# Kernel optimization log

Measured on AMD Instinct MI355X. Metric: run time of the kernel, lower is better.

The kernel has to match this reference:

```python
import jax, jax.numpy as jnp
import numpy as np

N_NODES = 100000
F_IN = 512
HIDDEN = 64
N_CLASS = 40
N_EDGES = 3200000


def gcn_conv(x, src, dst, deg_inv_sqrt, W, b, n_nodes):
    # PyG GCNConv: linear transform, then deg^{-1/2} A_hat deg^{-1/2} aggregation, then bias
    h = x @ W  # [N, out]
    norm = deg_inv_sqrt[src] * deg_inv_sqrt[dst]  # [E+N] (includes self-loops)
    msg = h[src] * norm[:, None]  # gather + scale
    out = jax.ops.segment_sum(msg, dst, num_segments=n_nodes)  # scatter-add
    return out + b


def setup_inputs() -> dict:
    key = jax.random.key(0)
    k1, k2, k3, k4, k5 = jax.random.split(key, 5)
    x = jax.random.normal(k1, (N_NODES, F_IN), dtype=jnp.float32)
    edge_index = jax.random.randint(k2, (2, N_EDGES), 0, N_NODES, dtype=jnp.int64)
    # Glorot-style init for GCN weights
    W1 = jax.random.normal(k3, (F_IN, HIDDEN), dtype=jnp.float32) / np.sqrt(F_IN)
    b1 = jnp.zeros((HIDDEN,), dtype=jnp.float32)
    W2 = jax.random.normal(k4, (HIDDEN, N_CLASS), dtype=jnp.float32) / np.sqrt(HIDDEN)
    b2 = jnp.zeros((N_CLASS,), dtype=jnp.float32)
    return {"x": x, "edge_index": edge_index, "W1": W1, "b1": b1, "W2": W2, "b2": b2}


def reference(x, edge_index, W1, b1, W2, b2):
    n = x.shape[0]
    loops = jnp.arange(n, dtype=edge_index.dtype)
    src = jnp.concatenate([edge_index[0], loops])  # add self-loops (GCNConv default)
    dst = jnp.concatenate([edge_index[1], loops])
    deg = jax.ops.segment_sum(jnp.ones_like(dst, dtype=x.dtype), dst, num_segments=n)
    deg_inv_sqrt = jnp.where(deg > 0, jax.lax.rsqrt(deg), 0.0)
    h = gcn_conv(x, src, dst, deg_inv_sqrt, W1, b1, n)
    h = jax.nn.relu(h)  # dropout treated as eval-mode identity
    x_out = gcn_conv(h, src, dst, deg_inv_sqrt, W2, b2, n)
    return jax.nn.log_softmax(x_out, axis=1), x_out
```

## Files before the change

### kernel.cpp

```cpp
#include <hip/hip_runtime.h>
#include <math.h>

#define N_NODES 100000
#define F_IN    512
#define HIDDEN  64
#define N_CLASS 40
#define N_EDGES 3200000
#define NB      782
#define CAP     6144
#define EPB     8192
#define NPB     391

typedef int EIdx;

typedef __attribute__((ext_vector_type(8))) short short8;
typedef __attribute__((ext_vector_type(4))) float f32x4;
typedef __attribute__((ext_vector_type(4))) unsigned uint4v;

__device__ inline short f2bf(float f) {
    unsigned u = __builtin_bit_cast(unsigned, f);
    unsigned r = u + 0x7FFFu + ((u >> 16) & 1u);
    return (short)(r >> 16);
}

__device__ inline unsigned cvtpk(float lo, float hi) {
    unsigned r;
    asm("v_cvt_pk_bf16_f32 %0, %1, %2" : "=v"(r) : "v"(lo), "v"(hi));
    return r;
}

__device__ inline float bflo(unsigned w) { return __builtin_bit_cast(float, w << 16); }
__device__ inline float bfhi(unsigned w) { return __builtin_bit_cast(float, w & 0xFFFF0000u); }

__global__ __launch_bounds__(256) void binit_kernel(int* __restrict__ bcur) {
    int i = blockIdx.x * 256 + threadIdx.x;
    if (i < NB) bcur[i] = i * CAP;
}

__global__ __launch_bounds__(256) void part1_kernel(const EIdx* __restrict__ src,
                                                    const EIdx* __restrict__ dst,
                                                    int* __restrict__ bcur,
                                                    unsigned* __restrict__ bpacked) {
    __shared__ int hist[NB];
    __shared__ int excl[NB];
    __shared__ int cur[NB];
    __shared__ int delta[NB];
    __shared__ int stmp[256];
    __shared__ unsigned spk[EPB];
    __shared__ unsigned short bid[EPB];
    int t = threadIdx.x;
    int e0 = blockIdx.x * EPB;
    int dreg[32];
    for (int j = t; j < NB; j += 256) hist[j] = 0;
    __syncthreads();
#pragma unroll
    for (int k = 0; k < 32; ++k) {
        int e = e0 + k * 256 + t;
        dreg[k] = (e < N_EDGES) ? dst[e] : -1;
        if (dreg[k] >= 0) atomicAdd(&hist[dreg[k] >> 7], 1);
    }
    __syncthreads();
    {
        int i0 = 4 * t;
        int v0 = (i0 < NB) ? hist[i0] : 0;
        int v1 = (i0 + 1 < NB) ? hist[i0 + 1] : 0;
        int v2 = (i0 + 2 < NB) ? hist[i0 + 2] : 0;
        int v3 = (i0 + 3 < NB) ? hist[i0 + 3] : 0;
        int s = v0 + v1 + v2 + v3;
        stmp[t] = s;
        __syncthreads();
        for (int o = 1; o < 256; o <<= 1) {
            int a = (t >= o) ? stmp[t - o] : 0;
            __syncthreads();
            stmp[t] += a;
            __syncthreads();
        }
        int E = stmp[t] - s;
        if (i0 < NB) excl[i0] = E;
        if (i0 + 1 < NB) excl[i0 + 1] = E + v0;
        if (i0 + 2 < NB) excl[i0 + 2] = E + v0 + v1;
        if (i0 + 3 < NB) excl[i0 + 3] = E + v0 + v1 + v2;
    }
    __syncthreads();
    for (int j = t; j < NB; j += 256) {
        int h = hist[j];
        int rsv = h ? atomicAdd(&bcur[j], h) : 0;
        delta[j] = rsv - excl[j];
        cur[j] = excl[j];
    }
    __syncthreads();
#pragma unroll
    for (int k = 0; k < 32; ++k) {
        int d = dreg[k];
        if (d >= 0) {
            int e = e0 + k * 256 + t;
            int s = src[e];
            int b = d >> 7;
            int p = atomicAdd(&cur[b], 1);
            spk[p] = ((unsigned)(d & 127) << 20) | (unsigned)s;
            bid[p] = (unsigned short)b;
        }
    }
    __syncthreads();
    int cnt = N_EDGES - e0;
    if (cnt > EPB) cnt = EPB;
    for (int i = t; i < cnt; i += 256) {
        int bb = bid[i];
        int pos = i + delta[bb];
        if (pos < (bb + 1) * CAP) bpacked[pos] = spk[i];
    }
}

__global__ __launch_bounds__(256) void part2_kernel(const int* __restrict__ bcur,
                                                    const unsigned* __restrict__ bpacked,
                                                    int* __restrict__ csr_src,
                                                    unsigned* __restrict__ rowmeta,
                                                    float* __restrict__ dis) {
    __shared__ unsigned ent[CAP];
    __shared__ int hist[128];
    __shared__ int stmp[128];
    __shared__ int cur[128];
    int t = threadIdx.x;
    int bk = blockIdx.x;
    int base = bk * CAP;
    int cnt = bcur[bk] - base;
    if (cnt > CAP) cnt = CAP;
    if (t < 128) hist[t] = 0;
    __syncthreads();
    for (int i = t; i < cnt; i += 256) {
        unsigned p = bpacked[base + i];
        ent[i] = p;
        atomicAdd(&hist[p >> 20], 1);
    }
    __syncthreads();
    if (t < 128) stmp[t] = hist[t];
    __syncthreads();
    for (int o = 1; o < 128; o <<= 1) {
        int a = (t >= o && t < 128) ? stmp[t - o] : 0;
        __syncthreads();
        if (t < 128) stmp[t] += a;
        __syncthreads();
    }
    if (t < 128) {
        int ex = stmp[t] - hist[t];
        cur[t] = ex;
        int n = (bk << 7) + t;
        if (n < N_NODES) {
            rowmeta[n] = (unsigned)(base + ex) | ((unsigned)hist[t] << 23);
            dis[n] = rsqrtf((float)(hist[t] + 1));
        }
    }
    __syncthreads();
    for (int i = t; i < cnt; i += 256) {
        unsigned p = ent[i];
        int p2 = atomicAdd(&cur[p >> 20], 1);
        csr_src[base + p2] = (int)(p & 0xFFFFFu);
    }
}

__global__ __launch_bounds__(256) void wprep_kernel(const float* __restrict__ W,
                                                    short* __restrict__ Wbf) {
    int idx = blockIdx.x * 256 + threadIdx.x;
    int k = idx >> 6, col = idx & 63;
    Wbf[col * F_IN + (k ^ ((col & 7) << 3))] = f2bf(W[idx]);
}

__global__ __launch_bounds__(256) void gemm1_mfma_kernel(const float* __restrict__ x,
                                                         const short* __restrict__ Wbf,
                                                         const float* __restrict__ dis,
                                                         unsigned* __restrict__ h1b) {
    __shared__ short Wt[HIDDEN * 128];
    __shared__ short xs[128 * 40];
    int tid = threadIdx.x;
    int wave = tid >> 6, lane = tid & 63;
    int r0 = blockIdx.x * 128;
    int wr0 = r0 + wave * 32;
    int lrow = lane & 15;
    int lk = (lane >> 4) * 8;
    int bswz = (lane & 7) << 3;

    f32x4 acc[2][4];
#pragma unroll
    for (int m = 0; m < 2; ++m)
#pragma unroll
        for (int n = 0; n < 4; ++n) acc[m][n] = (f32x4)0.0f;

    int srow = 0, schunk = 0;
    {
        int idx0 = tid;
        srow = idx0 >> 3;
        schunk = idx0 & 7;
    }
    int grow[4];
#pragma unroll
    for (int i = 0; i < 4; ++i) {
        int r = r0 + srow + i * 32;
        grow[i] = (r < N_NODES) ? r : (N_NODES - 1);
    }

    float4 xr[4];
#pragma unroll
    for (int i = 0; i < 4; ++i)
        xr[i] = *reinterpret_cast<const float4*>(x + (size_t)grow[i] * F_IN + 4 * schunk);

    const short8* Wv = (const short8*)Wbf;
    short8* Lv = (short8*)Wt;

    for (int ks = 0; ks < 16; ++ks) {
        int kg = ks * 32;
        __syncthreads();
#pragma unroll
        for (int i = 0; i < 4; ++i) {
            uint2 u = {cvtpk(xr[i].x, xr[i].y), cvtpk(xr[i].z, xr[i].w)};
            *reinterpret_cast<uint2*>(&xs[(srow + i * 32) * 40 + 4 * schunk]) = u;
        }
        if ((kg & 127) == 0) {
            int q = kg >> 7;
            for (int i = tid; i < 1024; i += 256) {
                int col = i >> 4, kc = i & 15;
                Lv[i] = Wv[col * 64 + q * 16 + kc];
            }
        }
        __syncthreads();
        if (ks < 15) {
            int kn = kg + 32;
#pragma unroll
            for (int i = 0; i < 4; ++i)
                xr[i] = *reinterpret_cast<const float4*>(x + (size_t)grow[i] * F_IN + kn + 4 * schunk);
        }
        int k0loc = kg & 127;
        short8 a0 = *reinterpret_cast<const short8*>(&xs[(wave * 32 + lrow) * 40 + lk]);
        short8 a1 = *reinterpret_cast<const short8*>(&xs[(wave * 32 + 16 + lrow) * 40 + lk]);
        short8 b[4];
#pragma unroll
        for (int n = 0; n < 4; ++n) {
            int c = n * 16 + lrow;
            b[n] = *reinterpret_cast<const short8*>(&Wt[c * 128 + ((k0loc + lk) ^ bswz)]);
        }
#pragma unroll
        for (int n = 0; n < 4; ++n) {
            acc[0][n] = __builtin_amdgcn_mfma_f32_16x16x32_bf16(a0, b[n], acc[0][n], 0, 0, 0);
            acc[1][n] = __builtin_amdgcn_mfma_f32_16x16x32_bf16(a1, b[n], acc[1][n], 0, 0, 0);
        }
    }

    int crow = (lane >> 4) * 4, ccol = lane & 15;
    bool evenc = (ccol & 1) == 0;
#pragma unroll
    for (int m = 0; m < 2; ++m) {
#pragma unroll
        for (int j = 0; j < 4; ++j) {
            int rr = wr0 + m * 16 + crow + j;
            int rs = (rr < N_NODES) ? rr : (N_NODES - 1);
            float ds = dis[rs];
            float v[4], vn[4];
#pragma unroll
            for (int n = 0; n < 4; ++n) v[n] = acc[m][n][j] * ds;
#pragma unroll
            for (int n = 0; n < 4; ++n) vn[n] = __shfl_xor(v[n], 1);
            if (rr < N_NODES && evenc) {
#pragma unroll
                for (int n = 0; n < 4; ++n)
                    h1b[(size_t)rr * 32 + ((n * 16 + ccol) >> 1)] = cvtpk(v[n], vn[n]);
            }
        }
    }
}

__global__ __launch_bounds__(256) void gather1_gemm2_kernel(const unsigned* __restrict__ h1b,
                                                            const unsigned* __restrict__ rowmeta,
                                                            const int* __restrict__ csr_src,
                                                            const float* __restrict__ dis,
                                                            const float* __restrict__ b1,
                                                            const float* __restrict__ W2,
                                                            unsigned* __restrict__ h2b) {
    __shared__ float W2s[HIDDEN * N_CLASS];
    __shared__ float aggs[4 * HIDDEN];
    int tid = threadIdx.x;
    for (int i = tid; i < HIDDEN * N_CLASS; i += 256) W2s[i] = W2[i];

    int wave = tid >> 6, lane = tid & 63;
    int n = blockIdx.x * 4 + wave;
    int g = lane >> 4, l = lane & 15;
    unsigned meta = rowmeta[n];
    int i = (int)(meta & 0x7FFFFFu);
    int i1 = i + (int)(meta >> 23);
    float ax = 0.f, ay = 0.f, az = 0.f, aw = 0.f;
    if (g == 0) {
        uint2 v = *reinterpret_cast<const uint2*>(h1b + (size_t)n * 32 + 2 * l);
        ax = bflo(v.x); ay = bfhi(v.x); az = bflo(v.y); aw = bfhi(v.y);
    }
    for (; i + 15 < i1; i += 16) {
        int s0 = csr_src[i + g], s1 = csr_src[i + 4 + g];
        int s2 = csr_src[i + 8 + g], s3 = csr_src[i + 12 + g];
        uint2 r0 = *reinterpret_cast<const uint2*>(h1b + (size_t)s0 * 32 + 2 * l);
        uint2 r1 = *reinterpret_cast<const uint2*>(h1b + (size_t)s1 * 32 + 2 * l);
        uint2 r2 = *reinterpret_cast<const uint2*>(h1b + (size_t)s2 * 32 + 2 * l);
        uint2 r3 = *reinterpret_cast<const uint2*>(h1b + (size_t)s3 * 32 + 2 * l);
        ax += (bflo(r0.x) + bflo(r1.x)) + (bflo(r2.x) + bflo(r3.x));
        ay += (bfhi(r0.x) + bfhi(r1.x)) + (bfhi(r2.x) + bfhi(r3.x));
        az += (bflo(r0.y) + bflo(r1.y)) + (bflo(r2.y) + bflo(r3.y));
        aw += (bfhi(r0.y) + bfhi(r1.y)) + (bfhi(r2.y) + bfhi(r3.y));
    }
    for (; i < i1; i += 4) {
        if (i + g < i1) {
            int s = csr_src[i + g];
            uint2 r = *reinterpret_cast<const uint2*>(h1b + (size_t)s * 32 + 2 * l);
            ax += bflo(r.x); ay += bfhi(r.x); az += bflo(r.y); aw += bfhi(r.y);
        }
    }
    ax += __shfl_xor(ax, 16); ax += __shfl_xor(ax, 32);
    ay += __shfl_xor(ay, 16); ay += __shfl_xor(ay, 32);
    az += __shfl_xor(az, 16); az += __shfl_xor(az, 32);
    aw += __shfl_xor(aw, 16); aw += __shfl_xor(aw, 32);
    float ds = dis[n];
    if (g == 0) {
        float4 bb = *reinterpret_cast<const float4*>(b1 + 4 * l);
        float4 o = {fmaxf(fmaf(ax, ds, bb.x), 0.f), fmaxf(fmaf(ay, ds, bb.y), 0.f),
                    fmaxf(fmaf(az, ds, bb.z), 0.f), fmaxf(fmaf(aw, ds, bb.w), 0.f)};
        *reinterpret_cast<float4*>(&aggs[wave * HIDDEN + 4 * l]) = o;
    }
    __syncthreads();
    int c = lane;
    float out = 0.f;
    if (c < N_CLASS) {
#pragma unroll 8
        for (int k = 0; k < HIDDEN; ++k)
            out = fmaf(aggs[wave * HIDDEN + k], W2s[k * N_CLASS + c], out);
        out *= ds;
    }
    float outn = __shfl_xor(out, 1);
    if (c < N_CLASS && (c & 1) == 0)
        h2b[(size_t)n * 20 + (c >> 1)] = cvtpk(out, outn);
}

__global__ __launch_bounds__(256) void gather2_kernel(const unsigned* __restrict__ h2b,
                                                      const unsigned* __restrict__ rowmeta,
                                                      const int* __restrict__ csr_src,
                                                      const float* __restrict__ dis,
                                                      const float* __restrict__ b,
                                                      float* __restrict__ xout,
                                                      float* __restrict__ out_ls) {
    int n = blockIdx.x * 4 + (threadIdx.x >> 6);
    int lane = threadIdx.x & 63;
    int g = lane >> 4, l = lane & 15;
    bool al = l < 10;
    unsigned meta = rowmeta[n];
    int i = (int)(meta & 0x7FFFFFu);
    int i1 = i + (int)(meta >> 23);
    float ax = 0.f, ay = 0.f, az = 0.f, aw = 0.f;
    if (g == 0 && al) {
        uint2 v = *reinterpret_cast<const uint2*>(h2b + (size_t)n * 20 + 2 * l);
        ax = bflo(v.x); ay = bfhi(v.x); az = bflo(v.y); aw = bfhi(v.y);
    }
    for (; i + 15 < i1; i += 16) {
        int s0 = csr_src[i + g], s1 = csr_src[i + 4 + g];
        int s2 = csr_src[i + 8 + g], s3 = csr_src[i + 12 + g];
        if (al) {
            uint2 r0 = *reinterpret_cast<const uint2*>(h2b + (size_t)s0 * 20 + 2 * l);
            uint2 r1 = *reinterpret_cast<const uint2*>(h2b + (size_t)s1 * 20 + 2 * l);
            uint2 r2 = *reinterpret_cast<const uint2*>(h2b + (size_t)s2 * 20 + 2 * l);
            uint2 r3 = *reinterpret_cast<const uint2*>(h2b + (size_t)s3 * 20 + 2 * l);
            ax += (bflo(r0.x) + bflo(r1.x)) + (bflo(r2.x) + bflo(r3.x));
            ay += (bfhi(r0.x) + bfhi(r1.x)) + (bfhi(r2.x) + bfhi(r3.x));
            az += (bflo(r0.y) + bflo(r1.y)) + (bflo(r2.y) + bflo(r3.y));
            aw += (bfhi(r0.y) + bfhi(r1.y)) + (bfhi(r2.y) + bfhi(r3.y));
        }
    }
    for (; i < i1; i += 4) {
        if (al && i + g < i1) {
            int s = csr_src[i + g];
            uint2 r = *reinterpret_cast<const uint2*>(h2b + (size_t)s * 20 + 2 * l);
            ax += bflo(r.x); ay += bfhi(r.x); az += bflo(r.y); aw += bfhi(r.y);
        }
    }
    ax += __shfl_xor(ax, 16); ax += __shfl_xor(ax, 32);
    ay += __shfl_xor(ay, 16); ay += __shfl_xor(ay, 32);
    az += __shfl_xor(az, 16); az += __shfl_xor(az, 32);
    aw += __shfl_xor(aw, 16); aw += __shfl_xor(aw, 32);

    float ds = dis[n];
    float vx = 0.f, vy = 0.f, vz = 0.f, vw = 0.f;
    if (al) {
        float4 bb = *reinterpret_cast<const float4*>(b + 4 * l);
        vx = fmaf(ax, ds, bb.x); vy = fmaf(ay, ds, bb.y);
        vz = fmaf(az, ds, bb.z); vw = fmaf(aw, ds, bb.w);
    }
    float mx = al ? fmaxf(fmaxf(vx, vy), fmaxf(vz, vw)) : -INFINITY;
#pragma unroll
    for (int o = 8; o > 0; o >>= 1) mx = fmaxf(mx, __shfl_xor(mx, o));
    float e = al ? (expf(vx - mx) + expf(vy - mx)) + (expf(vz - mx) + expf(vw - mx)) : 0.0f;
    float sum = e;
#pragma unroll
    for (int o = 8; o > 0; o >>= 1) sum += __shfl_xor(sum, o);
    if (g == 0 && al) {
        float ls = mx + logf(sum);
        float4 xo = {vx, vy, vz, vw};
        float4 lo = {vx - ls, vy - ls, vz - ls, vw - ls};
        *reinterpret_cast<float4*>(xout + (size_t)n * N_CLASS + 4 * l) = xo;
        *reinterpret_cast<float4*>(out_ls + (size_t)n * N_CLASS + 4 * l) = lo;
    }
}

extern "C" void kernel_launch(void* const* d_in, const int* in_sizes, int n_in,
                              void* d_out, int out_size, void* d_ws, size_t ws_size,
                              hipStream_t stream) {
    const float* x  = (const float*)d_in[0];
    const EIdx*  ei = (const EIdx*)d_in[1];
    const float* W1 = (const float*)d_in[2];
    const float* b1 = (const float*)d_in[3];
    const float* W2 = (const float*)d_in[4];
    const float* b2 = (const float*)d_in[5];
    const EIdx* src = ei;
    const EIdx* dst = ei + N_EDGES;

    float* out_ls = (float*)d_out;
    float* x_out  = out_ls + (size_t)N_NODES * N_CLASS;

    char* w = (char*)d_ws;
    int*      bcur    = (int*)w;       w += 1024 * 4;
    float*    dis     = (float*)w;     w += 100352 * 4;
    unsigned* rowmeta = (unsigned*)w;  w += 100352 * 4;
    short*    Wbf     = (short*)w;     w += (size_t)F_IN * HIDDEN * 2;
    unsigned* bpacked = (unsigned*)w;
    unsigned* h1b     = (unsigned*)w;  w += (size_t)NB * CAP * 4;
    int*      csr_src = (int*)w;       w += (size_t)NB * CAP * 4;
    unsigned* h2b     = (unsigned*)w;  w += (size_t)N_NODES * 20 * 4;

    const int B = 256;
    int gW  = N_NODES / 4;
    int gM1 = (N_NODES + 127) / 128;

    binit_kernel<<<4, B, 0, stream>>>(bcur);
    part1_kernel<<<NPB, B, 0, stream>>>(src, dst, bcur, bpacked);
    part2_kernel<<<NB, B, 0, stream>>>(bcur, bpacked, csr_src, rowmeta, dis);
    wprep_kernel<<<(F_IN * HIDDEN) / B, B, 0, stream>>>(W1, Wbf);

    gemm1_mfma_kernel<<<gM1, B, 0, stream>>>(x, Wbf, dis, h1b);
    gather1_gemm2_kernel<<<gW, B, 0, stream>>>(h1b, rowmeta, csr_src, dis, b1, W2, h2b);

    gather2_kernel<<<gW, B, 0, stream>>>(h2b, rowmeta, csr_src, dis, b2, x_out, out_ls);
}
```

Before: 303.0 us.

## Remap gathers to eight lanes per node and split out a standalone GEMM2

Both neighbour-aggregation kernels now give each node an 8-lane group and 32 nodes per block. Each lane loads a 16-byte slice of a neighbour row and walks all edges itself, four at a time. This replaces the old scheme of one wave per node with edges split across lane groups, which then needed cross-group shuffle reductions. The layer-1 aggregation no longer applies W2 in shared memory. It writes an fp32 aggregated buffer, and a new per-thread GEMM2 kernel reads it back, holding 40 accumulators per row, to produce the bf16 layer-2 features. The remap is meant to raise memory-level parallelism and remove reductions, but unfusing adds an extra round trip of about 25 MB through global memory and one more kernel launch.

```diff
diff --git a/kernel.cpp b/kernel.cpp
--- a/kernel.cpp
+++ b/kernel.cpp
@@ -185,12 +185,8 @@
 #pragma unroll
         for (int n = 0; n < 4; ++n) acc[m][n] = (f32x4)0.0f;
 
-    int srow = 0, schunk = 0;
-    {
-        int idx0 = tid;
-        srow = idx0 >> 3;
-        schunk = idx0 & 7;
-    }
+    int srow = tid >> 3;
+    int schunk = tid & 7;
     int grow[4];
 #pragma unroll
     for (int i = 0; i < 4; ++i) {
@@ -267,138 +263,170 @@
     }
 }
 
-__global__ __launch_bounds__(256) void gather1_gemm2_kernel(const unsigned* __restrict__ h1b,
-                                                            const unsigned* __restrict__ rowmeta,
-                                                            const int* __restrict__ csr_src,
-                                                            const float* __restrict__ dis,
-                                                            const float* __restrict__ b1,
-                                                            const float* __restrict__ W2,
-                                                            unsigned* __restrict__ h2b) {
-    __shared__ float W2s[HIDDEN * N_CLASS];
-    __shared__ float aggs[4 * HIDDEN];
+__global__ __launch_bounds__(256) void gather1_kernel(const unsigned* __restrict__ h1b,
+                                                      const unsigned* __restrict__ rowmeta,
+                                                      const int* __restrict__ csr_src,
+                                                      const float* __restrict__ dis,
+                                                      const float* __restrict__ b1,
+                                                      float* __restrict__ out) {
     int tid = threadIdx.x;
-    for (int i = tid; i < HIDDEN * N_CLASS; i += 256) W2s[i] = W2[i];
-
-    int wave = tid >> 6, lane = tid & 63;
-    int n = blockIdx.x * 4 + wave;
-    int g = lane >> 4, l = lane & 15;
+    int n = blockIdx.x * 32 + (tid >> 3);
+    int l = tid & 7;
     unsigned meta = rowmeta[n];
-    int i = (int)(meta & 0x7FFFFFu);
-    int i1 = i + (int)(meta >> 23);
-    float ax = 0.f, ay = 0.f, az = 0.f, aw = 0.f;
-    if (g == 0) {
-        uint2 v = *reinterpret_cast<const uint2*>(h1b + (size_t)n * 32 + 2 * l);
-        ax = bflo(v.x); ay = bfhi(v.x); az = bflo(v.y); aw = bfhi(v.y);
-    }
-    for (; i + 15 < i1; i += 16) {
-        int s0 = csr_src[i + g], s1 = csr_src[i + 4 + g];
-        int s2 = csr_src[i + 8 + g], s3 = csr_src[i + 12 + g];
-        uint2 r0 = *reinterpret_cast<const uint2*>(h1b + (size_t)s0 * 32 + 2 * l);
-        uint2 r1 = *reinterpret_cast<const uint2*>(h1b + (size_t)s1 * 32 + 2 * l);
-        uint2 r2 = *reinterpret_cast<const uint2*>(h1b + (size_t)s2 * 32 + 2 * l);
-        uint2 r3 = *reinterpret_cast<const uint2*>(h1b + (size_t)s3 * 32 + 2 * l);
-        ax += (bflo(r0.x) + bflo(r1.x)) + (bflo(r2.x) + bflo(r3.x));
-        ay += (bfhi(r0.x) + bfhi(r1.x)) + (bfhi(r2.x) + bfhi(r3.x));
-        az += (bflo(r0.y) + bflo(r1.y)) + (bflo(r2.y) + bflo(r3.y));
-        aw += (bfhi(r0.y) + bfhi(r1.y)) + (bfhi(r2.y) + bfhi(r3.y));
-    }
-    for (; i < i1; i += 4) {
-        if (i + g < i1) {
-            int s = csr_src[i + g];
-            uint2 r = *reinterpret_cast<const uint2*>(h1b + (size_t)s * 32 + 2 * l);
-            ax += bflo(r.x); ay += bfhi(r.x); az += bflo(r.y); aw += bfhi(r.y);
-        }
-    }
-    ax += __shfl_xor(ax, 16); ax += __shfl_xor(ax, 32);
-    ay += __shfl_xor(ay, 16); ay += __shfl_xor(ay, 32);
-    az += __shfl_xor(az, 16); az += __shfl_xor(az, 32);
-    aw += __shfl_xor(aw, 16); aw += __shfl_xor(aw, 32);
+    int base = (int)(meta & 0x7FFFFFu);
+    int deg = (int)(meta >> 23);
+    const unsigned* rowp = h1b + 4 * l;
+    uint4 v = *reinterpret_cast<const uint4*>(h1b + (size_t)n * 32 + 4 * l);
+    float a0 = bflo(v.x), a1 = bfhi(v.x), a2 = bflo(v.y), a3 = bfhi(v.y);
+    float a4 = bflo(v.z), a5 = bfhi(v.z), a6 = bflo(v.w), a7 = bfhi(v.w);
+    int e = 0;
+    for (; e + 3 < deg; e += 4) {
+        int s0 = csr_src[base + e],     s1 = csr_src[base + e + 1];
+        int s2 = csr_src[base + e + 2], s3 = csr_src[base + e + 3];
+        uint4 r0 = *reinterpret_cast<const uint4*>(rowp + (size_t)s0 * 32);
+        uint4 r1 = *reinterpret_cast<const uint4*>(rowp + (size_t)s1 * 32);
+        uint4 r2 = *reinterpret_cast<const uint4*>(rowp + (size_t)s2 * 32);
+        uint4 r3 = *reinterpret_cast<const uint4*>(rowp + (size_t)s3 * 32);
+        a0 += (bflo(r0.x) + bflo(r1.x)) + (bflo(r2.x) + bflo(r3.x));
+        a1 += (bfhi(r0.x) + bfhi(r1.x)) + (bfhi(r2.x) + bfhi(r3.x));
+        a2 += (bflo(r0.y) + bflo(r1.y)) + (bflo(r2.y) + bflo(r3.y));
+        a3 += (bfhi(r0.y) + bfhi(r1.y)) + (bfhi(r2.y) + bfhi(r3.y));
+        a4 += (bflo(r0.z) + bflo(r1.z)) + (bflo(r2.z) + bflo(r3.z));
+        a5 += (bfhi(r0.z) + bfhi(r1.z)) + (bfhi(r2.z) + bfhi(r3.z));
+        a6 += (bflo(r0.w) + bflo(r1.w)) + (bflo(r2.w) + bflo(r3.w));
+        a7 += (bfhi(r0.w) + bfhi(r1.w)) + (bfhi(r2.w) + bfhi(r3.w));
+    }
+    for (; e < deg; ++e) {
+        int s = csr_src[base + e];
+        uint4 r = *reinterpret_cast<const uint4*>(rowp + (size_t)s * 32);
+        a0 += bflo(r.x); a1 += bfhi(r.x); a2 += bflo(r.y); a3 += bfhi(r.y);
+        a4 += bflo(r.z); a5 += bfhi(r.z); a6 += bflo(r.w); a7 += bfhi(r.w);
+    }
     float ds = dis[n];
-    if (g == 0) {
-        float4 bb = *reinterpret_cast<const float4*>(b1 + 4 * l);
-        float4 o = {fmaxf(fmaf(ax, ds, bb.x), 0.f), fmaxf(fmaf(ay, ds, bb.y), 0.f),
-                    fmaxf(fmaf(az, ds, bb.z), 0.f), fmaxf(fmaf(aw, ds, bb.w), 0.f)};
-        *reinterpret_cast<float4*>(&aggs[wave * HIDDEN + 4 * l]) = o;
-    }
-    __syncthreads();
-    int c = lane;
-    float out = 0.f;
-    if (c < N_CLASS) {
-#pragma unroll 8
-        for (int k = 0; k < HIDDEN; ++k)
-            out = fmaf(aggs[wave * HIDDEN + k], W2s[k * N_CLASS + c], out);
-        out *= ds;
-    }
-    float outn = __shfl_xor(out, 1);
-    if (c < N_CLASS && (c & 1) == 0)
-        h2b[(size_t)n * 20 + (c >> 1)] = cvtpk(out, outn);
+    float4 bL = *reinterpret_cast<const float4*>(b1 + 8 * l);
+    float4 bH = *reinterpret_cast<const float4*>(b1 + 8 * l + 4);
+    float4 oL = {fmaxf(fmaf(a0, ds, bL.x), 0.f), fmaxf(fmaf(a1, ds, bL.y), 0.f),
+                 fmaxf(fmaf(a2, ds, bL.z), 0.f), fmaxf(fmaf(a3, ds, bL.w), 0.f)};
+    float4 oH = {fmaxf(fmaf(a4, ds, bH.x), 0.f), fmaxf(fmaf(a5, ds, bH.y), 0.f),
+                 fmaxf(fmaf(a6, ds, bH.z), 0.f), fmaxf(fmaf(a7, ds, bH.w), 0.f)};
+    float* op = out + (size_t)n * HIDDEN + 8 * l;
+    *reinterpret_cast<float4*>(op) = oL;
+    *reinterpret_cast<float4*>(op + 4) = oH;
+}
+
+__global__ __launch_bounds__(256) void gemm2_kernel(const float* __restrict__ x,
+                                                    const float* __restrict__ W,
+                                                    const float* __restrict__ dis,
+                                                    unsigned* __restrict__ h2b) {
+    int r = blockIdx.x * 256 + threadIdx.x;
+    if (r >= N_NODES) return;
+    float acc[N_CLASS];
+#pragma unroll
+    for (int j = 0; j < N_CLASS; ++j) acc[j] = 0.0f;
+    const float* xr = x + (size_t)r * HIDDEN;
+    for (int k0 = 0; k0 < HIDDEN; k0 += 4) {
+        float4 xv = *reinterpret_cast<const float4*>(xr + k0);
+        const float* wk = W + (size_t)k0 * N_CLASS;
+#pragma unroll
+        for (int j = 0; j < N_CLASS; ++j) {
+            acc[j] = fmaf(xv.x, wk[j], acc[j]);
+            acc[j] = fmaf(xv.y, wk[N_CLASS + j], acc[j]);
+            acc[j] = fmaf(xv.z, wk[2 * N_CLASS + j], acc[j]);
+            acc[j] = fmaf(xv.w, wk[3 * N_CLASS + j], acc[j]);
+        }
+    }
+    float ds = dis[r];
+    unsigned* hr = h2b + (size_t)r * 20;
+#pragma unroll
+    for (int q = 0; q < 5; ++q) {
+        uint4v o = {cvtpk(acc[8 * q] * ds,     acc[8 * q + 1] * ds),
+                    cvtpk(acc[8 * q + 2] * ds, acc[8 * q + 3] * ds),
+                    cvtpk(acc[8 * q + 4] * ds, acc[8 * q + 5] * ds),
+                    cvtpk(acc[8 * q + 6] * ds, acc[8 * q + 7] * ds)};
+        *reinterpret_cast<uint4v*>(hr + 4 * q) = o;
+    }
 }
 
 __global__ __launch_bounds__(256) void gather2_kernel(const unsigned* __restrict__ h2b,
                                                       const unsigned* __restrict__ rowmeta,
                                                       const int* __restrict__ csr_src,
                                                       const float* __restrict__ dis,
-                                                      const float* __restrict__ b,
+                                                      const float* __restrict__ b2,
                                                       float* __restrict__ xout,
                                                       float* __restrict__ out_ls) {
-    int n = blockIdx.x * 4 + (threadIdx.x >> 6);
-    int lane = threadIdx.x & 63;
-    int g = lane >> 4, l = lane & 15;
-    bool al = l < 10;
+    int tid = threadIdx.x;
+    int n = blockIdx.x * 32 + (tid >> 3);
+    int l = tid & 7;
+    bool act = l < 5;
     unsigned meta = rowmeta[n];
-    int i = (int)(meta & 0x7FFFFFu);
-    int i1 = i + (int)(meta >> 23);
-    float ax = 0.f, ay = 0.f, az = 0.f, aw = 0.f;
-    if (g == 0 && al) {
-        uint2 v = *reinterpret_cast<const uint2*>(h2b + (size_t)n * 20 + 2 * l);
-        ax = bflo(v.x); ay = bfhi(v.x); az = bflo(v.y); aw = bfhi(v.y);
-    }
-    for (; i + 15 < i1; i += 16) {
-        int s0 = csr_src[i + g], s1 = csr_src[i + 4 + g];
-        int s2 = csr_src[i + 8 + g], s3 = csr_src[i + 12 + g];
-        if (al) {
-            uint2 r0 = *reinterpret_cast<const uint2*>(h2b + (size_t)s0 * 20 + 2 * l);
-            uint2 r1 = *reinterpret_cast<const uint2*>(h2b + (size_t)s1 * 20 + 2 * l);
-            uint2 r2 = *reinterpret_cast<const uint2*>(h2b + (size_t)s2 * 20 + 2 * l);
-            uint2 r3 = *reinterpret_cast<const uint2*>(h2b + (size_t)s3 * 20 + 2 * l);
-            ax += (bflo(r0.x) + bflo(r1.x)) + (bflo(r2.x) + bflo(r3.x));
-            ay += (bfhi(r0.x) + bfhi(r1.x)) + (bfhi(r2.x) + bfhi(r3.x));
-            az += (bflo(r0.y) + bflo(r1.y)) + (bflo(r2.y) + bflo(r3.y));
-            aw += (bfhi(r0.y) + bfhi(r1.y)) + (bfhi(r2.y) + bfhi(r3.y));
-        }
-    }
-    for (; i < i1; i += 4) {
-        if (al && i + g < i1) {
-            int s = csr_src[i + g];
-            uint2 r = *reinterpret_cast<const uint2*>(h2b + (size_t)s * 20 + 2 * l);
-            ax += bflo(r.x); ay += bfhi(r.x); az += bflo(r.y); aw += bfhi(r.y);
-        }
-    }
-    ax += __shfl_xor(ax, 16); ax += __shfl_xor(ax, 32);
-    ay += __shfl_xor(ay, 16); ay += __shfl_xor(ay, 32);
-    az += __shfl_xor(az, 16); az += __shfl_xor(az, 32);
-    aw += __shfl_xor(aw, 16); aw += __shfl_xor(aw, 32);
-
+    int base = (int)(meta & 0x7FFFFFu);
+    int deg = (int)(meta >> 23);
+    const unsigned* rowp = h2b + 4 * l;
+    float a0 = 0.f, a1 = 0.f, a2 = 0.f, a3 = 0.f, a4 = 0.f, a5 = 0.f, a6 = 0.f, a7 = 0.f;
+    if (act) {
+        uint4 v = *reinterpret_cast<const uint4*>(h2b + (size_t)n * 20 + 4 * l);
+        a0 = bflo(v.x); a1 = bfhi(v.x); a2 = bflo(v.y); a3 = bfhi(v.y);
+        a4 = bflo(v.z); a5 = bfhi(v.z); a6 = bflo(v.w); a7 = bfhi(v.w);
+    }
+    int e = 0;
+    for (; e + 3 < deg; e += 4) {
+        int s0 = csr_src[base + e],     s1 = csr_src[base + e + 1];
+        int s2 = csr_src[base + e + 2], s3 = csr_src[base + e + 3];
+        if (act) {
+            uint4 r0 = *reinterpret_cast<const uint4*>(rowp + (size_t)s0 * 20);
+            uint4 r1 = *reinterpret_cast<const uint4*>(rowp + (size_t)s1 * 20);
+            uint4 r2 = *reinterpret_cast<const uint4*>(rowp + (size_t)s2 * 20);
+            uint4 r3 = *reinterpret_cast<const uint4*>(rowp + (size_t)s3 * 20);
+            a0 += (bflo(r0.x) + bflo(r1.x)) + (bflo(r2.x) + bflo(r3.x));
+            a1 += (bfhi(r0.x) + bfhi(r1.x)) + (bfhi(r2.x) + bfhi(r3.x));
+            a2 += (bflo(r0.y) + bflo(r1.y)) + (bflo(r2.y) + bflo(r3.y));
+            a3 += (bfhi(r0.y) + bfhi(r1.y)) + (bfhi(r2.y) + bfhi(r3.y));
+            a4 += (bflo(r0.z) + bflo(r1.z)) + (bflo(r2.z) + bflo(r3.z));
+            a5 += (bfhi(r0.z) + bfhi(r1.z)) + (bfhi(r2.z) + bfhi(r3.z));
+            a6 += (bflo(r0.w) + bflo(r1.w)) + (bflo(r2.w) + bflo(r3.w));
+            a7 += (bfhi(r0.w) + bfhi(r1.w)) + (bfhi(r2.w) + bfhi(r3.w));
+        }
+    }
+    for (; e < deg; ++e) {
+        int s = csr_src[base + e];
+        if (act) {
+            uint4 r = *reinterpret_cast<const uint4*>(rowp + (size_t)s * 20);
+            a0 += bflo(r.x); a1 += bfhi(r.x); a2 += bflo(r.y); a3 += bfhi(r.y);
+            a4 += bflo(r.z); a5 += bfhi(r.z); a6 += bflo(r.w); a7 += bfhi(r.w);
+        }
+    }
     float ds = dis[n];
-    float vx = 0.f, vy = 0.f, vz = 0.f, vw = 0.f;
-    if (al) {
-        float4 bb = *reinterpret_cast<const float4*>(b + 4 * l);
-        vx = fmaf(ax, ds, bb.x); vy = fmaf(ay, ds, bb.y);
-        vz = fmaf(az, ds, bb.z); vw = fmaf(aw, ds, bb.w);
-    }
-    float mx = al ? fmaxf(fmaxf(vx, vy), fmaxf(vz, vw)) : -INFINITY;
-#pragma unroll
-    for (int o = 8; o > 0; o >>= 1) mx = fmaxf(mx, __shfl_xor(mx, o));
-    float e = al ? (expf(vx - mx) + expf(vy - mx)) + (expf(vz - mx) + expf(vw - mx)) : 0.0f;
-    float sum = e;
-#pragma unroll
-    for (int o = 8; o > 0; o >>= 1) sum += __shfl_xor(sum, o);
-    if (g == 0 && al) {
+    float v0 = 0.f, v1 = 0.f, v2 = 0.f, v3 = 0.f, v4 = 0.f, v5 = 0.f, v6 = 0.f, v7 = 0.f;
+    if (act) {
+        float4 bL = *reinterpret_cast<const float4*>(b2 + 8 * l);
+        float4 bH = *reinterpret_cast<const float4*>(b2 + 8 * l + 4);
+        v0 = fmaf(a0, ds, bL.x); v1 = fmaf(a1, ds, bL.y);
+        v2 = fmaf(a2, ds, bL.z); v3 = fmaf(a3, ds, bL.w);
+        v4 = fmaf(a4, ds, bH.x); v5 = fmaf(a5, ds, bH.y);
+        v6 = fmaf(a6, ds, bH.z); v7 = fmaf(a7, ds, bH.w);
+    }
+    float mx = act ? fmaxf(fmaxf(fmaxf(v0, v1), fmaxf(v2, v3)),
+                           fmaxf(fmaxf(v4, v5), fmaxf(v6, v7))) : -INFINITY;
+    mx = fmaxf(mx, __shfl_xor(mx, 1));
+    mx = fmaxf(mx, __shfl_xor(mx, 2));
+    mx = fmaxf(mx, __shfl_xor(mx, 4));
+    float sum = act ? ((expf(v0 - mx) + expf(v1 - mx)) + (expf(v2 - mx) + expf(v3 - mx))) +
+                      ((expf(v4 - mx) + expf(v5 - mx)) + (expf(v6 - mx) + expf(v7 - mx))) : 0.f;
+    sum += __shfl_xor(sum, 1);
+    sum += __shfl_xor(sum, 2);
+    sum += __shfl_xor(sum, 4);
+    if (act) {
         float ls = mx + logf(sum);
-        float4 xo = {vx, vy, vz, vw};
-        float4 lo = {vx - ls, vy - ls, vz - ls, vw - ls};
-        *reinterpret_cast<float4*>(xout + (size_t)n * N_CLASS + 4 * l) = xo;
-        *reinterpret_cast<float4*>(out_ls + (size_t)n * N_CLASS + 4 * l) = lo;
+        float* xp = xout + (size_t)n * N_CLASS + 8 * l;
+        float* lp = out_ls + (size_t)n * N_CLASS + 8 * l;
+        float4 xoL = {v0, v1, v2, v3};
+        float4 xoH = {v4, v5, v6, v7};
+        float4 loL = {v0 - ls, v1 - ls, v2 - ls, v3 - ls};
+        float4 loH = {v4 - ls, v5 - ls, v6 - ls, v7 - ls};
+        *reinterpret_cast<float4*>(xp) = xoL;
+        *reinterpret_cast<float4*>(xp + 4) = xoH;
+        *reinterpret_cast<float4*>(lp) = loL;
+        *reinterpret_cast<float4*>(lp + 4) = loH;
     }
 }
 
@@ -426,9 +454,11 @@
     unsigned* h1b     = (unsigned*)w;  w += (size_t)NB * CAP * 4;
     int*      csr_src = (int*)w;       w += (size_t)NB * CAP * 4;
     unsigned* h2b     = (unsigned*)w;  w += (size_t)N_NODES * 20 * 4;
+    float*    agg1    = (float*)w;     w += (size_t)N_NODES * HIDDEN * 4;
 
     const int B = 256;
-    int gW  = N_NODES / 4;
+    int gG  = N_NODES / 32;
+    int gN  = (N_NODES + B - 1) / B;
     int gM1 = (N_NODES + 127) / 128;
 
     binit_kernel<<<4, B, 0, stream>>>(bcur);
@@ -437,7 +467,8 @@
     wprep_kernel<<<(F_IN * HIDDEN) / B, B, 0, stream>>>(W1, Wbf);
 
     gemm1_mfma_kernel<<<gM1, B, 0, stream>>>(x, Wbf, dis, h1b);
-    gather1_gemm2_kernel<<<gW, B, 0, stream>>>(h1b, rowmeta, csr_src, dis, b1, W2, h2b);
-
-    gather2_kernel<<<gW, B, 0, stream>>>(h2b, rowmeta, csr_src, dis, b2, x_out, out_ls);
-}
+    gather1_kernel<<<gG, B, 0, stream>>>(h1b, rowmeta, csr_src, dis, b1, agg1);
+
+    gemm2_kernel<<<gN, B, 0, stream>>>(agg1, W2, dis, h2b);
+    gather2_kernel<<<gG, B, 0, stream>>>(h2b, rowmeta, csr_src, dis, b2, x_out, out_ls);
+}
```

New measurement: 273.5 us. 9.7% less time.
